# Kernel tuning notes

Hardware: AMD Instinct MI355X
Metric: run time of the kernel (lower is better)

## Reference

```python
import jax, jax.numpy as jnp
import numpy as np

D_MODEL = 256
NHEAD = 8
NLAYERS = 4
DFF = 1024
PATCH = 8
INPUT = 32
C = 2
DATA_DIM = C * PATCH * PATCH  # 128
P = (INPUT // PATCH) ** 2     # 16
NEG = -1.0e6                  # _neg_large_for_dtype(float32)
EPS = 1e-5


def _ln(x, w, b):
    m = x.mean(-1, keepdims=True)
    v = ((x - m) ** 2).mean(-1, keepdims=True)
    return (x - m) / jnp.sqrt(v + EPS) * w + b


def _forward(img_baseline, acq_dts_float, nan_token, pad_embed, emb_w, emb_b, spatial_pos,
             t_w1, t_b1, t_w2, t_b2, t_w3, t_b3,
             in_proj_w, in_proj_b, out_proj_w, out_proj_b,
             lin1_w, lin1_b, lin2_w, lin2_b, norm1_w, norm1_b, norm2_w, norm2_b,
             mean_w1, mean_b1, mean_w2, mean_b2, lv_w1, lv_b1, lv_w2, lv_b2):
    B, T, Cc, Hh, Ww = img_baseline.shape
    p = PATCH
    gh, gw = Hh // p, Ww // p
    L = T * P
    frame_pad = jnp.all(img_baseline == -9999.0, axis=(2, 3, 4))  # (B,T)
    nan_pix = jnp.isnan(img_baseline)
    token = jnp.clip(nan_token, -10.0, 10.0).reshape(1, 1, Cc, 1, 1)
    x = jnp.clip(jnp.where(nan_pix, token, img_baseline), -10.0, 10.0)

    def patchify(a):  # b t c (h ph)(w pw) -> b t (h w) (c ph pw)
        return a.reshape(B, T, Cc, gh, p, gw, p).transpose(0, 1, 3, 5, 2, 4, 6).reshape(B, T, P, Cc * p * p)

    xp = patchify(x)
    seq_nan = patchify(nan_pix).all(-1).reshape(B, L)
    seq_pad = jnp.broadcast_to(frame_pad[:, :, None], (B, T, P)).reshape(B, L)

    # temporal MLP embedding
    t_in = jnp.where(jnp.isnan(acq_dts_float), 0.0, acq_dts_float)[..., None]  # (B,T,1)
    h = jax.nn.relu(t_in @ t_w1.T + t_b1)
    h = jax.nn.relu(h @ t_w2.T + t_b2)
    temb = h @ t_w3.T + t_b3  # (B,T,D)

    z = xp @ emb_w.T + emb_b + spatial_pos + temb[:, :, None, :]  # (B,T,P,D)
    z = z.reshape(B, L, D_MODEL)
    z = jnp.where(seq_pad[..., None], pad_embed, z)  # masked_scatter of pad_embed

    # additive attention mask: rows with NaN/pad patches are fully masked except diagonal
    masked_rows = seq_nan | seq_pad
    mask = jnp.broadcast_to(jnp.where(masked_rows[:, :, None], NEG, 0.0), (B, L, L))
    eye = jnp.eye(L, dtype=bool)
    mask = jnp.where(eye[None, :, :] & masked_rows[:, :, None], 0.0, mask)
    # key_padding_mask merged additively on key columns
    mask = mask + jnp.where(seq_pad[:, None, :], NEG, 0.0)
    mask = mask[:, None, :, :]  # (B,1,L,L), shared across heads

    dh = D_MODEL // NHEAD
    scale = 1.0 / np.sqrt(dh).astype(np.float32)
    for l in range(NLAYERS):
        qkv = z @ in_proj_w[l].T + in_proj_b[l]
        q, k, v = jnp.split(qkv, 3, axis=-1)
        q = q.reshape(B, L, NHEAD, dh).transpose(0, 2, 1, 3)
        k = k.reshape(B, L, NHEAD, dh).transpose(0, 2, 1, 3)
        v = v.reshape(B, L, NHEAD, dh).transpose(0, 2, 1, 3)
        scores = jnp.einsum('bhqd,bhkd->bhqk', q, k) * scale + mask
        attn = jax.nn.softmax(scores, axis=-1)
        o = jnp.einsum('bhqk,bhkd->bhqd', attn, v).transpose(0, 2, 1, 3).reshape(B, L, D_MODEL)
        o = o @ out_proj_w[l].T + out_proj_b[l]
        z = _ln(z + o, norm1_w[l], norm1_b[l])
        ff = jax.nn.relu(z @ lin1_w[l].T + lin1_b[l]) @ lin2_w[l].T + lin2_b[l]
        z = _ln(z + ff, norm2_w[l], norm2_b[l])

    mean = jnp.clip(jax.nn.relu(z @ mean_w1.T + mean_b1) @ mean_w2.T + mean_b2, -10.0, 10.0)
    logvar = jnp.clip(jax.nn.relu(z @ lv_w1.T + lv_b1) @ lv_w2.T + lv_b2, -10.0, 5.0)

    def unpatch(a):  # b t (h w)(c ph pw) -> b t c (h ph)(w pw)
        return a.reshape(B, T, gh, gw, Cc, p, p).transpose(0, 1, 4, 2, 5, 3, 6).reshape(B, T, Cc, Hh, Ww)

    mean = unpatch(mean.reshape(B, T, P, DATA_DIM))
    logvar = unpatch(logvar.reshape(B, T, P, DATA_DIM))
    return mean[:, -1], logvar[:, -1]


def setup_inputs() -> dict:
    key = jax.random.key(0)
    ks = iter(jax.random.split(key, 48))

    def rn(shape, scale=0.02):
        return jax.random.normal(next(ks), shape, dtype=jnp.float32) * scale

    B, T = 4, 64
    z = lambda s: jnp.zeros(s, jnp.float32)
    return {
        'img_baseline': jax.random.normal(next(ks), (B, T, C, INPUT, INPUT), dtype=jnp.float32),
        'acq_dts_float': jax.random.uniform(next(ks), (B, T), dtype=jnp.float32) * 3000.0,
        'nan_token': rn((C,)),
        'pad_embed': rn((1, 1, D_MODEL)),
        'emb_w': rn((D_MODEL, DATA_DIM)),
        'emb_b': z((D_MODEL,)),
        'spatial_pos': rn((1, 1, P, D_MODEL)),
        't_w1': rn((64, 1)), 't_b1': z((64,)),
        't_w2': rn((128, 64)), 't_b2': z((128,)),
        't_w3': rn((D_MODEL, 128)), 't_b3': z((D_MODEL,)),
        'in_proj_w': rn((NLAYERS, 3 * D_MODEL, D_MODEL)),
        'in_proj_b': z((NLAYERS, 3 * D_MODEL)),
        'out_proj_w': rn((NLAYERS, D_MODEL, D_MODEL)),
        'out_proj_b': z((NLAYERS, D_MODEL)),
        'lin1_w': rn((NLAYERS, DFF, D_MODEL)), 'lin1_b': z((NLAYERS, DFF)),
        'lin2_w': rn((NLAYERS, D_MODEL, DFF)), 'lin2_b': z((NLAYERS, D_MODEL)),
        'norm1_w': jnp.ones((NLAYERS, D_MODEL), jnp.float32), 'norm1_b': z((NLAYERS, D_MODEL)),
        'norm2_w': jnp.ones((NLAYERS, D_MODEL), jnp.float32), 'norm2_b': z((NLAYERS, D_MODEL)),
        'mean_w1': rn((DFF, D_MODEL)), 'mean_b1': z((DFF,)),
        'mean_w2': rn((DATA_DIM, DFF)), 'mean_b2': z((DATA_DIM,)),
        'lv_w1': rn((DFF, D_MODEL)), 'lv_b1': z((DFF,)),
        'lv_w2': rn((DATA_DIM, DFF)), 'lv_b2': z((DATA_DIM,)),
    }


def reference(img_baseline, acq_dts_float, nan_token, pad_embed, emb_w, emb_b, spatial_pos,
              t_w1, t_b1, t_w2, t_b2, t_w3, t_b3,
              in_proj_w, in_proj_b, out_proj_w, out_proj_b,
              lin1_w, lin1_b, lin2_w, lin2_b, norm1_w, norm1_b, norm2_w, norm2_b,
              mean_w1, mean_b1, mean_w2, mean_b2, lv_w1, lv_b1, lv_w2, lv_b2):
    return _forward(img_baseline, acq_dts_float, nan_token, pad_embed, emb_w, emb_b, spatial_pos,
                    t_w1, t_b1, t_w2, t_b2, t_w3, t_b3,
                    in_proj_w, in_proj_b, out_proj_w, out_proj_b,
                    lin1_w, lin1_b, lin2_w, lin2_b, norm1_w, norm1_b, norm2_w, norm2_b,
                    mean_w1, mean_b1, mean_w2, mean_b2, lv_w1, lv_b1, lv_w2, lv_b2)
```

## Files before the change

### kernel.cpp

```cpp
#include <hip/hip_runtime.h>
#include <hip/hip_bf16.h>

#define D_MODEL 256
#define NHEAD 8
#define DH 32
#define NLAYERS 4
#define DFF 1024
#define CC 2
#define DATA_DIM 128
#define PP 16
#define TT 64
#define BB 4
#define LL 1024
#define NEGV -1000000.0f

typedef __bf16 bf16_t;
typedef __bf16 bf16x8 __attribute__((ext_vector_type(8)));
typedef __bf16 bf16x4 __attribute__((ext_vector_type(4)));
typedef float v4f __attribute__((ext_vector_type(4)));

__device__ __forceinline__ bool my_isnan(float v) {
    unsigned u = __float_as_uint(v);
    return (u & 0x7fffffffu) > 0x7f800000u;
}

__global__ void f2b_all_kernel(const float* __restrict__ s0, bf16_t* __restrict__ d0, int n0,
                               const float* __restrict__ s1, bf16_t* __restrict__ d1, int n1,
                               const float* __restrict__ s2, bf16_t* __restrict__ d2, int n2,
                               const float* __restrict__ s3, bf16_t* __restrict__ d3, int n3,
                               const float* __restrict__ s4, bf16_t* __restrict__ d4, int n4,
                               const float* __restrict__ s5, bf16_t* __restrict__ d5, int n5,
                               const float* __restrict__ s6, bf16_t* __restrict__ d6, int n6,
                               const float* __restrict__ s7, bf16_t* __restrict__ d7, int n7,
                               const float* __restrict__ s8, bf16_t* __restrict__ d8, int n8) {
    int i = (blockIdx.x * 256 + threadIdx.x) * 4;
    const float* s;
    bf16_t* d;
    if (i < n0) { s = s0; d = d0; }
    else if ((i -= n0) < n1) { s = s1; d = d1; }
    else if ((i -= n1) < n2) { s = s2; d = d2; }
    else if ((i -= n2) < n3) { s = s3; d = d3; }
    else if ((i -= n3) < n4) { s = s4; d = d4; }
    else if ((i -= n4) < n5) { s = s5; d = d5; }
    else if ((i -= n5) < n6) { s = s6; d = d6; }
    else if ((i -= n6) < n7) { s = s7; d = d7; }
    else if ((i -= n7) < n8) { s = s8; d = d8; }
    else return;
    float4 v = *(const float4*)(s + i);
    bf16x4 o = {(bf16_t)v.x, (bf16_t)v.y, (bf16_t)v.z, (bf16_t)v.w};
    *(bf16x4*)(d + i) = o;
}

__global__ void prep_frame_kernel(const float* __restrict__ img,
                                  const float* __restrict__ acq,
                                  const float* __restrict__ t_w1, const float* __restrict__ t_b1,
                                  const float* __restrict__ t_w2, const float* __restrict__ t_b2,
                                  const float* __restrict__ t_w3, const float* __restrict__ t_b3,
                                  float* __restrict__ temb, int* __restrict__ framepad) {
    int f = blockIdx.x;
    int tid = threadIdx.x;
    __shared__ float h1[64];
    __shared__ float h2[128];
    __shared__ int sAll;
    if (tid == 0) sAll = 1;
    __syncthreads();
    const float* fr = img + (size_t)f * (CC * 32 * 32);
    bool allpad = true;
    #pragma unroll
    for (int i = 0; i < 8; ++i) {
        float v = fr[tid + i * 256];
        allpad = allpad && (v == -9999.0f);
    }
    if (!allpad) sAll = 0;
    __syncthreads();
    if (tid == 0) framepad[f] = sAll;

    float t_in = acq[f];
    if (my_isnan(t_in)) t_in = 0.0f;
    if (tid < 64) h1[tid] = fmaxf(t_w1[tid] * t_in + t_b1[tid], 0.0f);
    __syncthreads();
    if (tid < 128) {
        float a = t_b2[tid];
        #pragma unroll 8
        for (int j = 0; j < 64; ++j) a += t_w2[tid * 64 + j] * h1[j];
        h2[tid] = fmaxf(a, 0.0f);
    }
    __syncthreads();
    {
        float a = t_b3[tid];
        #pragma unroll 8
        for (int j = 0; j < 128; ++j) a += t_w3[tid * 128 + j] * h2[j];
        temb[(size_t)f * D_MODEL + tid] = a;
    }
}

__global__ __launch_bounds__(256) void patchify_kernel(
    const float* __restrict__ img, const float* __restrict__ nan_token,
    const int* __restrict__ framepad,
    bf16_t* __restrict__ xpb, int* __restrict__ masked_rows,
    float* __restrict__ kmaskf) {
    int tid = threadIdx.x;
    int token = blockIdx.x * 2 + (tid >> 7);
    int dd = tid & 127;
    int l = token & 1023, b = token >> 10;
    int t = l >> 4, p = l & 15;
    int c = dd >> 6, pr = (dd >> 3) & 7, pc = dd & 7;
    int hh = (p >> 2) * 8 + pr, ww = (p & 3) * 8 + pc;
    float v = img[(((size_t)(b * TT + t) * CC + c) * 32 + hh) * 32 + ww];
    bool nanp = my_isnan(v);
    if (nanp) v = fminf(fmaxf(nan_token[c], -10.0f), 10.0f);
    v = fminf(fmaxf(v, -10.0f), 10.0f);
    xpb[(size_t)token * DATA_DIM + dd] = (bf16_t)v;

    __shared__ int wAll[4];
    unsigned long long bal = __ballot(nanp);
    if ((tid & 63) == 0) wAll[tid >> 6] = (bal == 0xFFFFFFFFFFFFFFFFull) ? 1 : 0;
    __syncthreads();
    if (tid < 2) {
        int tk = blockIdx.x * 2 + tid;
        int allnan = wAll[tid * 2] & wAll[tid * 2 + 1];
        int fp = framepad[tk >> 4];
        masked_rows[tk] = allnan | fp;
        kmaskf[tk] = fp ? NEGV : 0.0f;
    }
}

__global__ __launch_bounds__(256) void embed_gemm(
    const bf16_t* __restrict__ X, const bf16_t* __restrict__ W,
    const float* __restrict__ emb_b, const float* __restrict__ spatial,
    const float* __restrict__ temb, const float* __restrict__ pad_embed,
    const int* __restrict__ framepad,
    float* __restrict__ z, bf16_t* __restrict__ zb) {
    __shared__ __align__(16) bf16_t Xs[128 * 32];
    __shared__ __align__(16) bf16_t Ws[64 * 32];
    int tid = threadIdx.x;
    int wave = tid >> 6, lane = tid & 63;
    int quad = lane >> 4, l16 = lane & 15;
    int m0 = blockIdx.y * 128, n0 = blockIdx.x * 64;
    const int K = DATA_DIM, N = D_MODEL;

    v4f acc[2][4];
    #pragma unroll
    for (int i = 0; i < 2; ++i)
        #pragma unroll
        for (int j = 0; j < 4; ++j) acc[i][j] = (v4f){0.f, 0.f, 0.f, 0.f};

    int sr = tid >> 2, ss = tid & 3;
    for (int k0 = 0; k0 < K; k0 += 32) {
        uint4 a0 = *(const uint4*)(X + (size_t)(m0 + sr) * K + k0 + ss * 8);
        uint4 a1 = *(const uint4*)(X + (size_t)(m0 + 64 + sr) * K + k0 + ss * 8);
        uint4 b0 = *(const uint4*)(W + (size_t)(n0 + sr) * K + k0 + ss * 8);
        *(uint4*)(Xs + sr * 32 + ss * 8) = a0;
        *(uint4*)(Xs + (64 + sr) * 32 + ss * 8) = a1;
        *(uint4*)(Ws + sr * 32 + ss * 8) = b0;
        __syncthreads();
        bf16x8 af0 = *(const bf16x8*)(Xs + (wave * 32 + l16) * 32 + quad * 8);
        bf16x8 af1 = *(const bf16x8*)(Xs + (wave * 32 + 16 + l16) * 32 + quad * 8);
        #pragma unroll
        for (int nt = 0; nt < 4; ++nt) {
            bf16x8 bfr = *(const bf16x8*)(Ws + (nt * 16 + l16) * 32 + quad * 8);
            acc[0][nt] = __builtin_amdgcn_mfma_f32_16x16x32_bf16(af0, bfr, acc[0][nt], 0, 0, 0);
            acc[1][nt] = __builtin_amdgcn_mfma_f32_16x16x32_bf16(af1, bfr, acc[1][nt], 0, 0, 0);
        }
        __syncthreads();
    }

    #pragma unroll
    for (int mt = 0; mt < 2; ++mt)
        #pragma unroll
        for (int nt = 0; nt < 4; ++nt) {
            int col = n0 + nt * 16 + l16;
            #pragma unroll
            for (int reg = 0; reg < 4; ++reg) {
                int row = m0 + wave * 32 + mt * 16 + quad * 4 + reg;
                int frame = row >> 4, p = row & 15;
                float v;
                if (framepad[frame]) {
                    v = pad_embed[col];
                } else {
                    v = acc[mt][nt][reg] + emb_b[col] + spatial[p * N + col]
                      + temb[(size_t)frame * N + col];
                }
                z[(size_t)row * N + col] = v;
                zb[(size_t)row * N + col] = (bf16_t)v;
            }
        }
}

template <int MODE, int RELU>
__global__ __launch_bounds__(256) void gemm_mfma(
    const bf16_t* __restrict__ X, const bf16_t* __restrict__ W,
    const float* __restrict__ bias, bf16_t* __restrict__ Y,
    bf16_t* __restrict__ Vt, int M, int N, int K) {
    __shared__ __align__(16) bf16_t Xs[128 * 32];
    __shared__ __align__(16) bf16_t Ws[64 * 32];
    int tid = threadIdx.x;
    int wave = tid >> 6, lane = tid & 63;
    int quad = lane >> 4, l16 = lane & 15;
    int m0 = blockIdx.y * 128, n0 = blockIdx.x * 64;

    v4f acc[2][4];
    #pragma unroll
    for (int i = 0; i < 2; ++i)
        #pragma unroll
        for (int j = 0; j < 4; ++j) acc[i][j] = (v4f){0.f, 0.f, 0.f, 0.f};

    int sr = tid >> 2, ss = tid & 3;
    for (int k0 = 0; k0 < K; k0 += 32) {
        uint4 a0 = *(const uint4*)(X + (size_t)(m0 + sr) * K + k0 + ss * 8);
        uint4 a1 = *(const uint4*)(X + (size_t)(m0 + 64 + sr) * K + k0 + ss * 8);
        uint4 b0 = *(const uint4*)(W + (size_t)(n0 + sr) * K + k0 + ss * 8);
        *(uint4*)(Xs + sr * 32 + ss * 8) = a0;
        *(uint4*)(Xs + (64 + sr) * 32 + ss * 8) = a1;
        *(uint4*)(Ws + sr * 32 + ss * 8) = b0;
        __syncthreads();
        bf16x8 af0 = *(const bf16x8*)(Xs + (wave * 32 + l16) * 32 + quad * 8);
        bf16x8 af1 = *(const bf16x8*)(Xs + (wave * 32 + 16 + l16) * 32 + quad * 8);
        #pragma unroll
        for (int nt = 0; nt < 4; ++nt) {
            bf16x8 bfr = *(const bf16x8*)(Ws + (nt * 16 + l16) * 32 + quad * 8);
            acc[0][nt] = __builtin_amdgcn_mfma_f32_16x16x32_bf16(af0, bfr, acc[0][nt], 0, 0, 0);
            acc[1][nt] = __builtin_amdgcn_mfma_f32_16x16x32_bf16(af1, bfr, acc[1][nt], 0, 0, 0);
        }
        __syncthreads();
    }

    if constexpr (MODE == 1) {
        #pragma unroll
        for (int mt = 0; mt < 2; ++mt)
            #pragma unroll
            for (int nt = 0; nt < 4; ++nt) {
                int col = n0 + nt * 16 + l16;
                float bv = bias[col];
                #pragma unroll
                for (int reg = 0; reg < 4; ++reg) {
                    int row = m0 + wave * 32 + mt * 16 + quad * 4 + reg;
                    float v = acc[mt][nt][reg] + bv;
                    if (RELU) v = fmaxf(v, 0.0f);
                    Y[(size_t)row * N + col] = (bf16_t)v;
                }
            }
    } else {
        if (n0 < 512) {
            #pragma unroll
            for (int mt = 0; mt < 2; ++mt)
                #pragma unroll
                for (int nt = 0; nt < 4; ++nt) {
                    int col = n0 + nt * 16 + l16;
                    float bv = bias[col];
                    #pragma unroll
                    for (int reg = 0; reg < 4; ++reg) {
                        int row = m0 + wave * 32 + mt * 16 + quad * 4 + reg;
                        float v = acc[mt][nt][reg] + bv;
                        Y[(size_t)row * 768 + col] = (bf16_t)v;
                    }
                }
        } else {
            __shared__ __align__(16) bf16_t VT[64 * 136];
            #pragma unroll
            for (int mt = 0; mt < 2; ++mt)
                #pragma unroll
                for (int nt = 0; nt < 4; ++nt) {
                    int cl = nt * 16 + l16;
                    float bv = bias[n0 + cl];
                    #pragma unroll
                    for (int reg = 0; reg < 4; ++reg) {
                        int rl = wave * 32 + mt * 16 + quad * 4 + reg;
                        VT[cl * 136 + rl] = (bf16_t)(acc[mt][nt][reg] + bv);
                    }
                }
            __syncthreads();
            int b = m0 >> 10, l0m = m0 & 1023;
            int cl = tid >> 2;
            int rbase = (tid & 3) * 8;
            int cg = n0 + cl - 512;
            int h = cg >> 5, d = cg & 31;
            bf16_t* dst = Vt + (((size_t)(b * NHEAD + h)) * DH + d) * LL + l0m;
            #pragma unroll
            for (int u = 0; u < 4; ++u)
                *(uint4*)(dst + rbase + u * 32) = *(const uint4*)(VT + cl * 136 + rbase + u * 32);
        }
    }
}

__global__ __launch_bounds__(256) void gemm_small(
    const bf16_t* __restrict__ X, const bf16_t* __restrict__ W,
    const float* __restrict__ bias, float* __restrict__ Y,
    int M, int N, int K) {
    __shared__ __align__(16) bf16_t Xs[64 * 32];
    __shared__ __align__(16) bf16_t Ws[64 * 32];
    int tid = threadIdx.x;
    int wave = tid >> 6, lane = tid & 63;
    int quad = lane >> 4, l16 = lane & 15;
    int m0 = blockIdx.y * 64, n0 = blockIdx.x * 64;

    v4f acc[4];
    #pragma unroll
    for (int j = 0; j < 4; ++j) acc[j] = (v4f){0.f, 0.f, 0.f, 0.f};

    int sr = tid >> 2, ss = tid & 3;
    for (int k0 = 0; k0 < K; k0 += 32) {
        uint4 a0 = *(const uint4*)(X + (size_t)(m0 + sr) * K + k0 + ss * 8);
        uint4 b0 = *(const uint4*)(W + (size_t)(n0 + sr) * K + k0 + ss * 8);
        *(uint4*)(Xs + sr * 32 + ss * 8) = a0;
        *(uint4*)(Ws + sr * 32 + ss * 8) = b0;
        __syncthreads();
        bf16x8 af = *(const bf16x8*)(Xs + (wave * 16 + l16) * 32 + quad * 8);
        #pragma unroll
        for (int nt = 0; nt < 4; ++nt) {
            bf16x8 bfr = *(const bf16x8*)(Ws + (nt * 16 + l16) * 32 + quad * 8);
            acc[nt] = __builtin_amdgcn_mfma_f32_16x16x32_bf16(af, bfr, acc[nt], 0, 0, 0);
        }
        __syncthreads();
    }

    #pragma unroll
    for (int nt = 0; nt < 4; ++nt) {
        int col = n0 + nt * 16 + l16;
        float bv = bias[col];
        #pragma unroll
        for (int reg = 0; reg < 4; ++reg) {
            int row = m0 + wave * 16 + quad * 4 + reg;
            Y[(size_t)row * N + col] = acc[nt][reg] + bv;
        }
    }
}

__global__ __launch_bounds__(256) void attn_mfma(
    const bf16_t* __restrict__ qkvb, const bf16_t* __restrict__ Vt,
    const int* __restrict__ masked_rows, const float* __restrict__ kmaskf,
    bf16_t* __restrict__ Ob) {
    __shared__ __align__(16) bf16_t Ks[2][128 * 40];
    __shared__ __align__(16) bf16_t Vs[2][32 * 136];
    __shared__ __align__(16) float  Kms[2][128];
    __shared__ __align__(16) bf16_t Ps[4][16 * 136];

    int tid = threadIdx.x;
    int wave = tid >> 6, lane = tid & 63;
    int quad = lane >> 4, l16 = lane & 15;
    int bid = blockIdx.x;
    int h = bid & 7, b = (bid >> 3) & 3, qt = bid >> 5;
    int q0 = qt * 64 + wave * 16;
    const float scale = 0.17677669529663687f;

    bf16x8 qf = *(const bf16x8*)(qkvb + ((size_t)(b * LL) + q0 + l16) * 768 + h * DH + quad * 8);

    int mq[4];
    #pragma unroll
    for (int reg = 0; reg < 4; ++reg) mq[reg] = masked_rows[b * LL + q0 + quad * 4 + reg];

    float mrun[4], lrun[4];
    v4f oacc[2];
    #pragma unroll
    for (int reg = 0; reg < 4; ++reg) { mrun[reg] = -3.0e38f; lrun[reg] = 0.0f; }
    oacc[0] = (v4f){0.f, 0.f, 0.f, 0.f};
    oacc[1] = (v4f){0.f, 0.f, 0.f, 0.f};

    int kr = tid >> 1, kh = (tid & 1) * 16;
    int vd = tid >> 3, vs0 = (tid & 7) * 8;
    const bf16_t* Kbase = qkvb + (size_t)(b * LL) * 768 + 256 + h * DH;
    const bf16_t* Vbase = Vt + (((size_t)(b * NHEAD + h)) * DH) * LL;
    const float* kmbase = kmaskf + b * LL;

    uint4 ka, kb, va, vb;
    float kmg;
    #define LOADC(c)                                                            \
        do {                                                                    \
            int _k0 = (c) * 128;                                                \
            ka = *(const uint4*)(Kbase + (size_t)(_k0 + kr) * 768 + kh);        \
            kb = *(const uint4*)(Kbase + (size_t)(_k0 + kr) * 768 + kh + 8);    \
            va = *(const uint4*)(Vbase + (size_t)vd * LL + _k0 + vs0);          \
            vb = *(const uint4*)(Vbase + (size_t)vd * LL + _k0 + 64 + vs0);     \
            kmg = (tid < 128) ? kmbase[_k0 + tid] : 0.0f;                       \
        } while (0)
    #define WRITEBUF(buf)                                                       \
        do {                                                                    \
            *(uint4*)(Ks[(buf)] + kr * 40 + kh) = ka;                           \
            *(uint4*)(Ks[(buf)] + kr * 40 + kh + 8) = kb;                       \
            *(uint4*)(Vs[(buf)] + vd * 136 + vs0) = va;                         \
            *(uint4*)(Vs[(buf)] + vd * 136 + 64 + vs0) = vb;                    \
            if (tid < 128) Kms[(buf)][tid] = kmg;                               \
        } while (0)

    LOADC(0);
    WRITEBUF(0);
    LOADC(1);

    bf16_t* Pw = Ps[wave];
    for (int c = 0; c < 8; ++c) {
        __syncthreads();
        int cur = c & 1;
        if (c + 1 < 8) WRITEBUF(cur ^ 1);
        if (c + 2 < 8) LOADC(c + 2);

        int k0 = c * 128;
        const bf16_t* Kc = Ks[cur];
        const bf16_t* Vc = Vs[cur];
        const float* kmc = Kms[cur];

        v4f sf[8];
        #pragma unroll
        for (int nt = 0; nt < 8; ++nt) {
            bf16x8 kf = *(const bf16x8*)(Kc + (nt * 16 + l16) * 40 + quad * 8);
            v4f zf = (v4f){0.f, 0.f, 0.f, 0.f};
            sf[nt] = __builtin_amdgcn_mfma_f32_16x16x32_bf16(qf, kf, zf, 0, 0, 0);
        }

        float sv[8][4];
        #pragma unroll
        for (int nt = 0; nt < 8; ++nt) {
            int kg = k0 + nt * 16 + l16;
            float km = kmc[nt * 16 + l16];
            #pragma unroll
            for (int reg = 0; reg < 4; ++reg) {
                float v = sf[nt][reg] * scale + km;
                if (mq[reg] && (q0 + quad * 4 + reg != kg)) v += NEGV;
                sv[nt][reg] = v;
            }
        }

        float tm[4];
        #pragma unroll
        for (int reg = 0; reg < 4; ++reg) {
            float m = sv[0][reg];
            #pragma unroll
            for (int nt = 1; nt < 8; ++nt) m = fmaxf(m, sv[nt][reg]);
            tm[reg] = m;
        }
        #pragma unroll
        for (int off = 1; off < 16; off <<= 1)
            #pragma unroll
            for (int reg = 0; reg < 4; ++reg) tm[reg] = fmaxf(tm[reg], __shfl_xor(tm[reg], off));

        float alpha[4], psum[4];
        #pragma unroll
        for (int reg = 0; reg < 4; ++reg) {
            float mnew = fmaxf(mrun[reg], tm[reg]);
            alpha[reg] = __expf(mrun[reg] - mnew);
            mrun[reg] = mnew;
            float ps = 0.0f;
            #pragma unroll
            for (int nt = 0; nt < 8; ++nt) {
                float p = __expf(sv[nt][reg] - mnew);
                sv[nt][reg] = p;
                ps += p;
            }
            psum[reg] = ps;
        }
        #pragma unroll
        for (int off = 1; off < 16; off <<= 1)
            #pragma unroll
            for (int reg = 0; reg < 4; ++reg) psum[reg] += __shfl_xor(psum[reg], off);
        #pragma unroll
        for (int reg = 0; reg < 4; ++reg) {
            lrun[reg] = lrun[reg] * alpha[reg] + psum[reg];
            oacc[0][reg] *= alpha[reg];
            oacc[1][reg] *= alpha[reg];
        }

        #pragma unroll
        for (int nt = 0; nt < 8; ++nt)
            #pragma unroll
            for (int reg = 0; reg < 4; ++reg)
                Pw[(quad * 4 + reg) * 136 + nt * 16 + l16] = (bf16_t)sv[nt][reg];

        #pragma unroll
        for (int kt = 0; kt < 4; ++kt) {
            bf16x8 pf = *(const bf16x8*)(Pw + l16 * 136 + kt * 32 + quad * 8);
            #pragma unroll
            for (int nt2 = 0; nt2 < 2; ++nt2) {
                bf16x8 vf = *(const bf16x8*)(Vc + (nt2 * 16 + l16) * 136 + kt * 32 + quad * 8);
                oacc[nt2] = __builtin_amdgcn_mfma_f32_16x16x32_bf16(pf, vf, oacc[nt2], 0, 0, 0);
            }
        }
    }
    #undef LOADC
    #undef WRITEBUF

    #pragma unroll
    for (int nt2 = 0; nt2 < 2; ++nt2)
        #pragma unroll
        for (int reg = 0; reg < 4; ++reg) {
            size_t row = (size_t)(b * LL) + q0 + quad * 4 + reg;
            Ob[row * 256 + h * DH + nt2 * 16 + l16] = (bf16_t)(oacc[nt2][reg] / lrun[reg]);
        }
}

__global__ __launch_bounds__(256) void add_ln_kernel(
    float* __restrict__ z, const float* __restrict__ o,
    const float* __restrict__ w, const float* __restrict__ b,
    bf16_t* __restrict__ zb) {
    int wave = threadIdx.x >> 6, lane = threadIdx.x & 63;
    int row = blockIdx.x * 4 + wave;
    float4 x = ((const float4*)(z + (size_t)row * D_MODEL))[lane];
    float4 y = ((const float4*)(o + (size_t)row * D_MODEL))[lane];
    x.x += y.x; x.y += y.y; x.z += y.z; x.w += y.w;
    float s = x.x + x.y + x.z + x.w;
    #pragma unroll
    for (int off = 32; off > 0; off >>= 1) s += __shfl_xor(s, off);
    float mean = s * (1.0f / D_MODEL);
    float dx0 = x.x - mean, dx1 = x.y - mean, dx2 = x.z - mean, dx3 = x.w - mean;
    float sq = dx0 * dx0 + dx1 * dx1 + dx2 * dx2 + dx3 * dx3;
    #pragma unroll
    for (int off = 32; off > 0; off >>= 1) sq += __shfl_xor(sq, off);
    float inv = 1.0f / sqrtf(sq * (1.0f / D_MODEL) + 1e-5f);
    float4 wv = ((const float4*)w)[lane];
    float4 bv = ((const float4*)b)[lane];
    float4 r;
    r.x = dx0 * inv * wv.x + bv.x;
    r.y = dx1 * inv * wv.y + bv.y;
    r.z = dx2 * inv * wv.z + bv.z;
    r.w = dx3 * inv * wv.w + bv.w;
    ((float4*)(z + (size_t)row * D_MODEL))[lane] = r;
    bf16x4 rb = {(bf16_t)r.x, (bf16_t)r.y, (bf16_t)r.z, (bf16_t)r.w};
    *(bf16x4*)(zb + (size_t)row * D_MODEL + lane * 4) = rb;
}

__global__ __launch_bounds__(256) void head_h_kernel(
    const bf16_t* __restrict__ zb, const bf16_t* __restrict__ W1h,
    const float* __restrict__ B1f, bf16_t* __restrict__ hb) {
    __shared__ __align__(16) bf16_t Xs[64 * 32];
    __shared__ __align__(16) bf16_t Ws[64 * 32];
    int tid = threadIdx.x;
    int wave = tid >> 6, lane = tid & 63;
    int quad = lane >> 4, l16 = lane & 15;
    int n0 = blockIdx.x * 64;

    v4f acc[4];
    #pragma unroll
    for (int j = 0; j < 4; ++j) acc[j] = (v4f){0.f, 0.f, 0.f, 0.f};

    int sr = tid >> 2, ss = tid & 3;
    int gb = sr >> 4, gp = sr & 15;
    const bf16_t* xrow = zb + ((size_t)(gb * LL + (TT - 1) * PP + gp)) * D_MODEL;
    for (int k0 = 0; k0 < D_MODEL; k0 += 32) {
        *(uint4*)(Xs + sr * 32 + ss * 8) = *(const uint4*)(xrow + k0 + ss * 8);
        *(uint4*)(Ws + sr * 32 + ss * 8) =
            *(const uint4*)(W1h + (size_t)(n0 + sr) * D_MODEL + k0 + ss * 8);
        __syncthreads();
        bf16x8 af = *(const bf16x8*)(Xs + (wave * 16 + l16) * 32 + quad * 8);
        #pragma unroll
        for (int nt = 0; nt < 4; ++nt) {
            bf16x8 bfr = *(const bf16x8*)(Ws + (nt * 16 + l16) * 32 + quad * 8);
            acc[nt] = __builtin_amdgcn_mfma_f32_16x16x32_bf16(af, bfr, acc[nt], 0, 0, 0);
        }
        __syncthreads();
    }

    #pragma unroll
    for (int nt = 0; nt < 4; ++nt) {
        int col = n0 + nt * 16 + l16;
        float bv = B1f[col];
        #pragma unroll
        for (int reg = 0; reg < 4; ++reg) {
            int row = wave * 16 + quad * 4 + reg;
            hb[(size_t)row * DFF + col] = (bf16_t)fmaxf(acc[nt][reg] + bv, 0.0f);
        }
    }
}

__global__ __launch_bounds__(256) void head_out_kernel(
    const bf16_t* __restrict__ hb, const bf16_t* __restrict__ W2b,
    const float* __restrict__ mean_b2, const float* __restrict__ lv_b2,
    float* __restrict__ out) {
    __shared__ __align__(16) bf16_t hrow[DFF];
    int tid = threadIdx.x;
    int bid = blockIdx.x;
    int head = bid >> 7, rr = (bid >> 1) & 63, half = bid & 1;
    int b = rr >> 4, p = rr & 15;

    if (tid < 128)
        *(uint4*)(hrow + tid * 8) =
            *(const uint4*)(hb + ((size_t)head * 64 + rr) * DFF + tid * 8);
    __syncthreads();

    int ol = tid >> 2, quarter = tid & 3;
    int o = half * 64 + ol;
    const bf16_t* wrow = W2b + ((size_t)head * DATA_DIM + o) * DFF + quarter * 256;
    const bf16_t* hseg = hrow + quarter * 256;
    float acc = 0.0f;
    #pragma unroll 8
    for (int j = 0; j < 32; ++j) {
        bf16x8 w = *(const bf16x8*)(wrow + j * 8);
        bf16x8 hv = *(const bf16x8*)(hseg + j * 8);
        #pragma unroll
        for (int e = 0; e < 8; ++e) acc += (float)w[e] * (float)hv[e];
    }
    acc += __shfl_xor(acc, 1);
    acc += __shfl_xor(acc, 2);
    if (quarter == 0) {
        const float* B2 = head ? lv_b2 : mean_b2;
        float hi = head ? 5.0f : 10.0f;
        float v = fminf(fmaxf(acc + B2[o], -10.0f), hi);
        int c = o >> 6;
        int pr = (o >> 3) & 7, pc = o & 7;
        int hh = (p >> 2) * 8 + pr, ww = (p & 3) * 8 + pc;
        out[(size_t)head * 8192 + ((size_t)(b * CC + c)) * 1024 + hh * 32 + ww] = v;
    }
}

extern "C" void kernel_launch(void* const* d_in, const int* in_sizes, int n_in,
                              void* d_out, int out_size, void* d_ws, size_t ws_size,
                              hipStream_t stream) {
    const float* img        = (const float*)d_in[0];
    const float* acq        = (const float*)d_in[1];
    const float* nan_token  = (const float*)d_in[2];
    const float* pad_embed  = (const float*)d_in[3];
    const float* emb_w      = (const float*)d_in[4];
    const float* emb_b      = (const float*)d_in[5];
    const float* spatial    = (const float*)d_in[6];
    const float* t_w1       = (const float*)d_in[7];
    const float* t_b1       = (const float*)d_in[8];
    const float* t_w2       = (const float*)d_in[9];
    const float* t_b2       = (const float*)d_in[10];
    const float* t_w3       = (const float*)d_in[11];
    const float* t_b3       = (const float*)d_in[12];
    const float* in_proj_w  = (const float*)d_in[13];
    const float* in_proj_b  = (const float*)d_in[14];
    const float* out_proj_w = (const float*)d_in[15];
    const float* out_proj_b = (const float*)d_in[16];
    const float* lin1_w     = (const float*)d_in[17];
    const float* lin1_b     = (const float*)d_in[18];
    const float* lin2_w     = (const float*)d_in[19];
    const float* lin2_b     = (const float*)d_in[20];
    const float* norm1_w    = (const float*)d_in[21];
    const float* norm1_b    = (const float*)d_in[22];
    const float* norm2_w    = (const float*)d_in[23];
    const float* norm2_b    = (const float*)d_in[24];
    const float* mean_w1    = (const float*)d_in[25];
    const float* mean_b1    = (const float*)d_in[26];
    const float* mean_w2    = (const float*)d_in[27];
    const float* mean_b2    = (const float*)d_in[28];
    const float* lv_w1      = (const float*)d_in[29];
    const float* lv_b1      = (const float*)d_in[30];
    const float* lv_w2      = (const float*)d_in[31];
    const float* lv_b2      = (const float*)d_in[32];

    const int M = BB * LL;

    char* wsb = (char*)d_ws;
    float* z       = (float*)wsb;                    wsb += (size_t)M * D_MODEL * 4;
    float* tmpf    = (float*)wsb;                    wsb += (size_t)M * D_MODEL * 4;
    float* temb    = (float*)wsb;                    wsb += (size_t)BB * TT * D_MODEL * 4;
    float* kmaskf  = (float*)wsb;                    wsb += M * 4;
    int* framepad  = (int*)wsb;                      wsb += BB * TT * 4;
    int* masked    = (int*)wsb;                      wsb += M * 4;
    wsb = (char*)(((uintptr_t)wsb + 255) & ~(uintptr_t)255);
    bf16_t* zb     = (bf16_t*)wsb;                   wsb += (size_t)M * D_MODEL * 2;
    bf16_t* xpb    = (bf16_t*)wsb;                   wsb += (size_t)M * DATA_DIM * 2;
    bf16_t* qkvb   = (bf16_t*)wsb;                   wsb += (size_t)M * 768 * 2;
    bf16_t* VtG    = (bf16_t*)wsb;                   wsb += (size_t)M * D_MODEL * 2;
    bf16_t* attnb  = (bf16_t*)wsb;                   wsb += (size_t)M * D_MODEL * 2;
    bf16_t* ff1b   = (bf16_t*)wsb;                   wsb += (size_t)M * DFF * 2;
    bf16_t* inb    = (bf16_t*)wsb;                   wsb += (size_t)NLAYERS * 768 * D_MODEL * 2;
    bf16_t* outb   = (bf16_t*)wsb;                   wsb += (size_t)NLAYERS * D_MODEL * D_MODEL * 2;
    bf16_t* l1b    = (bf16_t*)wsb;                   wsb += (size_t)NLAYERS * DFF * D_MODEL * 2;
    bf16_t* l2b    = (bf16_t*)wsb;                   wsb += (size_t)NLAYERS * D_MODEL * DFF * 2;
    bf16_t* embwb  = (bf16_t*)wsb;                   wsb += (size_t)D_MODEL * DATA_DIM * 2;
    bf16_t* w1b    = (bf16_t*)wsb;                   wsb += (size_t)2 * DFF * D_MODEL * 2;
    bf16_t* w2b    = (bf16_t*)wsb;                   wsb += (size_t)2 * DATA_DIM * DFF * 2;
    bf16_t* hb     = (bf16_t*)wsb;                   wsb += (size_t)2 * 64 * DFF * 2;

    float* outF = (float*)d_out;

    {
        int n1 = NLAYERS * 768 * D_MODEL;
        int n2 = NLAYERS * D_MODEL * D_MODEL;
        int n3 = NLAYERS * DFF * D_MODEL;
        int n4 = NLAYERS * D_MODEL * DFF;
        int n5 = D_MODEL * DATA_DIM;
        int n6 = DFF * D_MODEL;
        int n7 = DFF * D_MODEL;
        int n8 = DATA_DIM * DFF;
        int n9 = DATA_DIM * DFF;
        int tot = n1 + n2 + n3 + n4 + n5 + n6 + n7 + n8 + n9;
        f2b_all_kernel<<<(tot / 4 + 255) / 256, 256, 0, stream>>>(
            in_proj_w, inb, n1, out_proj_w, outb, n2, lin1_w, l1b, n3,
            lin2_w, l2b, n4, emb_w, embwb, n5,
            mean_w1, w1b, n6, lv_w1, w1b + (size_t)DFF * D_MODEL, n7,
            mean_w2, w2b, n8, lv_w2, w2b + (size_t)DATA_DIM * DFF, n9);
    }

    prep_frame_kernel<<<BB * TT, 256, 0, stream>>>(img, acq, t_w1, t_b1, t_w2, t_b2,
                                                   t_w3, t_b3, temb, framepad);
    patchify_kernel<<<M / 2, 256, 0, stream>>>(img, nan_token, framepad, xpb, masked, kmaskf);
    embed_gemm<<<dim3(D_MODEL / 64, M / 128), 256, 0, stream>>>(
        xpb, embwb, emb_b, spatial, temb, pad_embed, framepad, z, zb);

    for (int l = 0; l < NLAYERS; ++l) {
        gemm_mfma<2, 0><<<dim3(768 / 64, M / 128), 256, 0, stream>>>(
            zb, inb + (size_t)l * 768 * D_MODEL, in_proj_b + (size_t)l * 768,
            qkvb, VtG, M, 768, D_MODEL);
        attn_mfma<<<BB * NHEAD * (LL / 64), 256, 0, stream>>>(qkvb, VtG, masked, kmaskf, attnb);
        gemm_small<<<dim3(D_MODEL / 64, M / 64), 256, 0, stream>>>(
            attnb, outb + (size_t)l * D_MODEL * D_MODEL, out_proj_b + (size_t)l * D_MODEL,
            tmpf, M, D_MODEL, D_MODEL);
        add_ln_kernel<<<M / 4, 256, 0, stream>>>(z, tmpf, norm1_w + l * D_MODEL,
                                                 norm1_b + l * D_MODEL, zb);
        gemm_mfma<1, 1><<<dim3(DFF / 64, M / 128), 256, 0, stream>>>(
            zb, l1b + (size_t)l * DFF * D_MODEL, lin1_b + (size_t)l * DFF,
            ff1b, nullptr, M, DFF, D_MODEL);
        gemm_small<<<dim3(D_MODEL / 64, M / 64), 256, 0, stream>>>(
            ff1b, l2b + (size_t)l * D_MODEL * DFF, lin2_b + (size_t)l * D_MODEL,
            tmpf, M, D_MODEL, DFF);
        add_ln_kernel<<<M / 4, 256, 0, stream>>>(z, tmpf, norm2_w + l * D_MODEL,
                                                 norm2_b + l * D_MODEL, zb);
    }

    head_h_kernel<<<DFF / 64, 256, 0, stream>>>(zb, w1b, mean_b1, hb);
    head_h_kernel<<<DFF / 64, 256, 0, stream>>>(
        zb, w1b + (size_t)DFF * D_MODEL, lv_b1, hb + (size_t)64 * DFF);
    head_out_kernel<<<256, 256, 0, stream>>>(hb, w2b, mean_b2, lv_b2, outF);
}
```

Measured before the change: 458.4 us.

## Use direct global-to-LDS loads, fuse residual add into GEMM, merge head launches

Replaces the register-staged global-to-shared tile copies in all GEMMs with global_load_lds direct-to-LDS transfers, which frees VGPRs and removes the separate shared-memory store instructions. The residual add moves from the layernorm kernel into the gemm_small epilogue, so the layernorm reads only one input tensor. The two head_h launches become a single launch over a 2D grid. Direct LDS loads rely on the lane-to-address layout matching the tile layout and give up manual control of when the loads are issued.

New measurement: 459.8 us. No clear change (+0.3%).

```diff
diff --git a/kernel.cpp b/kernel.cpp
--- a/kernel.cpp
+++ b/kernel.cpp
@@ -22,6 +22,12 @@
 __device__ __forceinline__ bool my_isnan(float v) {
     unsigned u = __float_as_uint(v);
     return (u & 0x7fffffffu) > 0x7f800000u;
+}
+
+__device__ __forceinline__ void gld16(bf16_t* l, const bf16_t* g) {
+    __builtin_amdgcn_global_load_lds(
+        (const __attribute__((address_space(1))) void*)g,
+        (__attribute__((address_space(3))) void*)l, 16, 0, 0);
 }
 
 __global__ void f2b_all_kernel(const float* __restrict__ s0, bf16_t* __restrict__ d0, int n0,
@@ -147,12 +153,9 @@
 
     int sr = tid >> 2, ss = tid & 3;
     for (int k0 = 0; k0 < K; k0 += 32) {
-        uint4 a0 = *(const uint4*)(X + (size_t)(m0 + sr) * K + k0 + ss * 8);
-        uint4 a1 = *(const uint4*)(X + (size_t)(m0 + 64 + sr) * K + k0 + ss * 8);
-        uint4 b0 = *(const uint4*)(W + (size_t)(n0 + sr) * K + k0 + ss * 8);
-        *(uint4*)(Xs + sr * 32 + ss * 8) = a0;
-        *(uint4*)(Xs + (64 + sr) * 32 + ss * 8) = a1;
-        *(uint4*)(Ws + sr * 32 + ss * 8) = b0;
+        gld16(Xs + tid * 8, X + (size_t)(m0 + sr) * K + k0 + ss * 8);
+        gld16(Xs + 2048 + tid * 8, X + (size_t)(m0 + 64 + sr) * K + k0 + ss * 8);
+        gld16(Ws + tid * 8, W + (size_t)(n0 + sr) * K + k0 + ss * 8);
         __syncthreads();
         bf16x8 af0 = *(const bf16x8*)(Xs + (wave * 32 + l16) * 32 + quad * 8);
         bf16x8 af1 = *(const bf16x8*)(Xs + (wave * 32 + 16 + l16) * 32 + quad * 8);
@@ -207,12 +210,9 @@
 
     int sr = tid >> 2, ss = tid & 3;
     for (int k0 = 0; k0 < K; k0 += 32) {
-        uint4 a0 = *(const uint4*)(X + (size_t)(m0 + sr) * K + k0 + ss * 8);
-        uint4 a1 = *(const uint4*)(X + (size_t)(m0 + 64 + sr) * K + k0 + ss * 8);
-        uint4 b0 = *(const uint4*)(W + (size_t)(n0 + sr) * K + k0 + ss * 8);
-        *(uint4*)(Xs + sr * 32 + ss * 8) = a0;
-        *(uint4*)(Xs + (64 + sr) * 32 + ss * 8) = a1;
-        *(uint4*)(Ws + sr * 32 + ss * 8) = b0;
+        gld16(Xs + tid * 8, X + (size_t)(m0 + sr) * K + k0 + ss * 8);
+        gld16(Xs + 2048 + tid * 8, X + (size_t)(m0 + 64 + sr) * K + k0 + ss * 8);
+        gld16(Ws + tid * 8, W + (size_t)(n0 + sr) * K + k0 + ss * 8);
         __syncthreads();
         bf16x8 af0 = *(const bf16x8*)(Xs + (wave * 32 + l16) * 32 + quad * 8);
         bf16x8 af1 = *(const bf16x8*)(Xs + (wave * 32 + 16 + l16) * 32 + quad * 8);
@@ -285,8 +285,8 @@
 
 __global__ __launch_bounds__(256) void gemm_small(
     const bf16_t* __restrict__ X, const bf16_t* __restrict__ W,
-    const float* __restrict__ bias, float* __restrict__ Y,
-    int M, int N, int K) {
+    const float* __restrict__ bias, const float* __restrict__ Zres,
+    float* __restrict__ Y, int M, int N, int K) {
     __shared__ __align__(16) bf16_t Xs[64 * 32];
     __shared__ __align__(16) bf16_t Ws[64 * 32];
     int tid = threadIdx.x;
@@ -300,10 +300,8 @@
 
     int sr = tid >> 2, ss = tid & 3;
     for (int k0 = 0; k0 < K; k0 += 32) {
-        uint4 a0 = *(const uint4*)(X + (size_t)(m0 + sr) * K + k0 + ss * 8);
-        uint4 b0 = *(const uint4*)(W + (size_t)(n0 + sr) * K + k0 + ss * 8);
-        *(uint4*)(Xs + sr * 32 + ss * 8) = a0;
-        *(uint4*)(Ws + sr * 32 + ss * 8) = b0;
+        gld16(Xs + tid * 8, X + (size_t)(m0 + sr) * K + k0 + ss * 8);
+        gld16(Ws + tid * 8, W + (size_t)(n0 + sr) * K + k0 + ss * 8);
         __syncthreads();
         bf16x8 af = *(const bf16x8*)(Xs + (wave * 16 + l16) * 32 + quad * 8);
         #pragma unroll
@@ -321,7 +319,7 @@
         #pragma unroll
         for (int reg = 0; reg < 4; ++reg) {
             int row = m0 + wave * 16 + quad * 4 + reg;
-            Y[(size_t)row * N + col] = acc[nt][reg] + bv;
+            Y[(size_t)row * N + col] = acc[nt][reg] + bv + Zres[(size_t)row * N + col];
         }
     }
 }
@@ -486,15 +484,13 @@
         }
 }
 
-__global__ __launch_bounds__(256) void add_ln_kernel(
-    float* __restrict__ z, const float* __restrict__ o,
+__global__ __launch_bounds__(256) void ln_kernel(
+    const float* __restrict__ tmpf, float* __restrict__ z,
     const float* __restrict__ w, const float* __restrict__ b,
     bf16_t* __restrict__ zb) {
     int wave = threadIdx.x >> 6, lane = threadIdx.x & 63;
     int row = blockIdx.x * 4 + wave;
-    float4 x = ((const float4*)(z + (size_t)row * D_MODEL))[lane];
-    float4 y = ((const float4*)(o + (size_t)row * D_MODEL))[lane];
-    x.x += y.x; x.y += y.y; x.z += y.z; x.w += y.w;
+    float4 x = ((const float4*)(tmpf + (size_t)row * D_MODEL))[lane];
     float s = x.x + x.y + x.z + x.w;
     #pragma unroll
     for (int off = 32; off > 0; off >>= 1) s += __shfl_xor(s, off);
@@ -517,14 +513,19 @@
 }
 
 __global__ __launch_bounds__(256) void head_h_kernel(
-    const bf16_t* __restrict__ zb, const bf16_t* __restrict__ W1h,
-    const float* __restrict__ B1f, bf16_t* __restrict__ hb) {
+    const bf16_t* __restrict__ zb, const bf16_t* __restrict__ W1b,
+    const float* __restrict__ mean_b1, const float* __restrict__ lv_b1,
+    bf16_t* __restrict__ hb) {
     __shared__ __align__(16) bf16_t Xs[64 * 32];
     __shared__ __align__(16) bf16_t Ws[64 * 32];
     int tid = threadIdx.x;
     int wave = tid >> 6, lane = tid & 63;
     int quad = lane >> 4, l16 = lane & 15;
+    int head = blockIdx.y;
     int n0 = blockIdx.x * 64;
+    const bf16_t* W1h = W1b + (size_t)head * DFF * D_MODEL;
+    const float* B1f = head ? lv_b1 : mean_b1;
+    bf16_t* hbh = hb + (size_t)head * 64 * DFF;
 
     v4f acc[4];
     #pragma unroll
@@ -534,9 +535,8 @@
     int gb = sr >> 4, gp = sr & 15;
     const bf16_t* xrow = zb + ((size_t)(gb * LL + (TT - 1) * PP + gp)) * D_MODEL;
     for (int k0 = 0; k0 < D_MODEL; k0 += 32) {
-        *(uint4*)(Xs + sr * 32 + ss * 8) = *(const uint4*)(xrow + k0 + ss * 8);
-        *(uint4*)(Ws + sr * 32 + ss * 8) =
-            *(const uint4*)(W1h + (size_t)(n0 + sr) * D_MODEL + k0 + ss * 8);
+        gld16(Xs + tid * 8, xrow + k0 + ss * 8);
+        gld16(Ws + tid * 8, W1h + (size_t)(n0 + sr) * D_MODEL + k0 + ss * 8);
         __syncthreads();
         bf16x8 af = *(const bf16x8*)(Xs + (wave * 16 + l16) * 32 + quad * 8);
         #pragma unroll
@@ -554,7 +554,7 @@
         #pragma unroll
         for (int reg = 0; reg < 4; ++reg) {
             int row = wave * 16 + quad * 4 + reg;
-            hb[(size_t)row * DFF + col] = (bf16_t)fmaxf(acc[nt][reg] + bv, 0.0f);
+            hbh[(size_t)row * DFF + col] = (bf16_t)fmaxf(acc[nt][reg] + bv, 0.0f);
         }
     }
 }
@@ -694,21 +694,19 @@
         attn_mfma<<<BB * NHEAD * (LL / 64), 256, 0, stream>>>(qkvb, VtG, masked, kmaskf, attnb);
         gemm_small<<<dim3(D_MODEL / 64, M / 64), 256, 0, stream>>>(
             attnb, outb + (size_t)l * D_MODEL * D_MODEL, out_proj_b + (size_t)l * D_MODEL,
-            tmpf, M, D_MODEL, D_MODEL);
-        add_ln_kernel<<<M / 4, 256, 0, stream>>>(z, tmpf, norm1_w + l * D_MODEL,
-                                                 norm1_b + l * D_MODEL, zb);
+            z, tmpf, M, D_MODEL, D_MODEL);
+        ln_kernel<<<M / 4, 256, 0, stream>>>(tmpf, z, norm1_w + l * D_MODEL,
+                                             norm1_b + l * D_MODEL, zb);
         gemm_mfma<1, 1><<<dim3(DFF / 64, M / 128), 256, 0, stream>>>(
             zb, l1b + (size_t)l * DFF * D_MODEL, lin1_b + (size_t)l * DFF,
             ff1b, nullptr, M, DFF, D_MODEL);
         gemm_small<<<dim3(D_MODEL / 64, M / 64), 256, 0, stream>>>(
             ff1b, l2b + (size_t)l * D_MODEL * DFF, lin2_b + (size_t)l * D_MODEL,
-            tmpf, M, D_MODEL, DFF);
-        add_ln_kernel<<<M / 4, 256, 0, stream>>>(z, tmpf, norm2_w + l * D_MODEL,
-                                                 norm2_b + l * D_MODEL, zb);
-    }
-
-    head_h_kernel<<<DFF / 64, 256, 0, stream>>>(zb, w1b, mean_b1, hb);
-    head_h_kernel<<<DFF / 64, 256, 0, stream>>>(
-        zb, w1b + (size_t)DFF * D_MODEL, lv_b1, hb + (size_t)64 * DFF);
+            z, tmpf, M, D_MODEL, DFF);
+        ln_kernel<<<M / 4, 256, 0, stream>>>(tmpf, z, norm2_w + l * D_MODEL,
+                                             norm2_b + l * D_MODEL, zb);
+    }
+
+    head_h_kernel<<<dim3(DFF / 64, 2), 256, 0, stream>>>(zb, w1b, mean_b1, lv_b1, hb);
     head_out_kernel<<<256, 256, 0, stream>>>(hb, w2b, mean_b2, lv_b2, outF);
 }
```
